# Kernel optimization log

Hardware: AMD Instinct MI355X
Metric: run time of the kernel (lower is better)

Reference implementation:

```python
import jax, jax.numpy as jnp
import numpy as np

B, T, C, H = 8, 1024, 1024, 16
Dh = C // H
EPS = 1e-5


def layernorm(x, g, b):
    m = jnp.mean(x, axis=-1, keepdims=True)
    v = jnp.mean((x - m) ** 2, axis=-1, keepdims=True)
    return g * (x - m) / jnp.sqrt(v + EPS) + b


def setup_inputs() -> dict:
    key = jax.random.key(0)
    ks = jax.random.split(key, 10)
    s = 0.02
    return {
        "x": jax.random.normal(ks[0], (B, T, C), jnp.float32),
        "Wq": jax.random.normal(ks[1], (H, C, Dh), jnp.float32) * s,
        "Wk": jax.random.normal(ks[2], (H, C, Dh), jnp.float32) * s,
        "Wv": jax.random.normal(ks[3], (H, C, Dh), jnp.float32) * s,
        "Wproj": jax.random.normal(ks[4], (C, C), jnp.float32) * s,
        "bproj": jnp.zeros((C,), jnp.float32),
        "W1": jax.random.normal(ks[5], (C, C), jnp.float32) * s,
        "b1": jnp.zeros((C,), jnp.float32),
        "W2": jax.random.normal(ks[6], (C, C), jnp.float32) * s,
        "b2": jnp.zeros((C,), jnp.float32),
        "g1": jnp.ones((C,), jnp.float32),
        "beta1": jnp.zeros((C,), jnp.float32),
        "g2": jnp.ones((C,), jnp.float32),
        "beta2": jnp.zeros((C,), jnp.float32),
    }


def reference(x, Wq, Wk, Wv, Wproj, bproj, W1, b1, W2, b2, g1, beta1, g2, beta2):
    # pre-LN multi-head causal self-attention + residual
    xn = layernorm(x, g1, beta1)
    q = jnp.einsum("btc,hcd->bhtd", xn, Wq)
    k = jnp.einsum("btc,hcd->bhtd", xn, Wk)
    v = jnp.einsum("btc,hcd->bhtd", xn, Wv)
    scores = jnp.einsum("bhtd,bhsd->bhts", q, k) * (Dh ** -0.5)
    causal = jnp.tril(jnp.ones((T, T), bool))  # [T,T]
    scores = jnp.where(causal, scores, -jnp.inf)
    wei = jax.nn.softmax(scores, axis=-1)
    attn = jnp.einsum("bhts,bhsd->bhtd", wei, v)
    attn = attn.transpose(0, 2, 1, 3).reshape(B, T, C)  # concat heads
    x = x + attn @ Wproj + bproj
    # pre-LN MLP (n_emb -> n_emb, ReLU, n_emb -> n_emb) + residual
    xn2 = layernorm(x, g2, beta2)
    h = jax.nn.relu(xn2 @ W1 + b1)
    x = x + h @ W2 + b2
    return x
```

## Files before the change

kernel.cpp:

```cpp
#include <hip/hip_runtime.h>
#include <hip/hip_bf16.h>

#define KDIM 1024

typedef __bf16  bf16x8  __attribute__((ext_vector_type(8)));
typedef float   floatx4 __attribute__((ext_vector_type(4)));

__device__ inline short f2bf(float f) {
    unsigned u = __float_as_uint(f);
    u += 0x7fffu + ((u >> 16) & 1u);
    return (short)(u >> 16);
}
__device__ inline float bf2f(short s) {
    return __uint_as_float(((unsigned)(unsigned short)s) << 16);
}
__device__ inline unsigned pk2bf(float x, float y) {
    __hip_bfloat162 h = __float22bfloat162_rn(make_float2(x, y));
    return *reinterpret_cast<unsigned*>(&h);
}
__device__ inline float exp2_hw(float x) {
    float r;
    __asm__("v_exp_f32 %0, %1" : "=v"(r) : "v"(x));
    return r;
}

__device__ inline floatx4 mfma16(bf16x8 a, bf16x8 b, floatx4 c) {
    return __builtin_amdgcn_mfma_f32_16x16x32_bf16(a, b, c, 0, 0, 0);
}

__device__ inline void load_lds16(const void* g, void* l) {
    __builtin_amdgcn_global_load_lds(
        (__attribute__((address_space(1))) void*)(unsigned long long)g,
        (__attribute__((address_space(3))) void*)(unsigned)(unsigned long long)l,
        16, 0, 0);
}

template <bool BF16IN>
__global__ __launch_bounds__(256) void ln_kernel(
    const void* __restrict__ xv, const float* __restrict__ g,
    const float* __restrict__ be, short* __restrict__ out)
{
    const int row = blockIdx.x, tid = threadIdx.x;
    float4 v;
    if constexpr (BF16IN) {
        const short4 s4 = ((const short4*)xv)[(size_t)row * 256 + tid];
        v.x = bf2f(s4.x); v.y = bf2f(s4.y); v.z = bf2f(s4.z); v.w = bf2f(s4.w);
    } else {
        v = ((const float4*)xv)[(size_t)row * 256 + tid];
    }
    float s  = v.x + v.y + v.z + v.w;
    float s2 = v.x * v.x + v.y * v.y + v.z * v.z + v.w * v.w;
    #pragma unroll
    for (int off = 32; off; off >>= 1) {
        s  += __shfl_down(s, off);
        s2 += __shfl_down(s2, off);
    }
    __shared__ float red1[4], red2[4];
    const int w = tid >> 6, lane = tid & 63;
    if (lane == 0) { red1[w] = s; red2[w] = s2; }
    __syncthreads();
    s  = red1[0] + red1[1] + red1[2] + red1[3];
    s2 = red2[0] + red2[1] + red2[2] + red2[3];
    const float mean = s * (1.0f / 1024.0f);
    const float var  = s2 * (1.0f / 1024.0f) - mean * mean;
    const float rstd = rsqrtf(var + 1e-5f);
    const float4 gg = ((const float4*)g)[tid];
    const float4 bb = ((const float4*)be)[tid];
    const unsigned o01 = pk2bf((v.x - mean) * rstd * gg.x + bb.x,
                               (v.y - mean) * rstd * gg.y + bb.y);
    const unsigned o23 = pk2bf((v.z - mean) * rstd * gg.z + bb.z,
                               (v.w - mean) * rstd * gg.w + bb.w);
    *(uint2*)(out + (size_t)row * 1024 + tid * 4) = make_uint2(o01, o23);
}

__global__ void pack_all(const float* __restrict__ Wq, const float* __restrict__ Wk,
                         const float* __restrict__ Wv, const float* __restrict__ Wproj,
                         const float* __restrict__ W1, const float* __restrict__ W2,
                         short* __restrict__ qkvT, short* __restrict__ projT,
                         short* __restrict__ w1T, short* __restrict__ w2T)
{
    __shared__ float tile[32][33];
    const int bx = blockIdx.x, c0 = blockIdx.y * 32;
    const int tx = threadIdx.x, ty = threadIdx.y;
    if (bx < 96) {
        const int n0 = bx * 32;
        const int grp = n0 >> 10;
        const float* W = (grp == 0) ? Wq : (grp == 1 ? Wk : Wv);
        const int nb = n0 & 1023, hh = nb >> 6, d0 = nb & 63;
        #pragma unroll
        for (int j = 0; j < 32; j += 8)
            tile[ty + j][tx] = W[hh * 65536 + (c0 + ty + j) * 64 + d0 + tx];
        __syncthreads();
        #pragma unroll
        for (int j = 0; j < 32; j += 8)
            qkvT[(size_t)(n0 + ty + j) * 1024 + c0 + tx] = f2bf(tile[tx][ty + j]);
    } else {
        const int which = (bx - 96) >> 5;
        const int n0 = ((bx - 96) & 31) * 32;
        const float* src = (which == 0) ? Wproj : (which == 1 ? W1 : W2);
        short* dst = (which == 0) ? projT : (which == 1 ? w1T : w2T);
        #pragma unroll
        for (int j = 0; j < 32; j += 8)
            tile[ty + j][tx] = src[(size_t)(c0 + ty + j) * 1024 + n0 + tx];
        __syncthreads();
        #pragma unroll
        for (int j = 0; j < 32; j += 8)
            dst[(size_t)(n0 + ty + j) * 1024 + c0 + tx] = f2bf(tile[tx][ty + j]);
    }
}

template <int EPI, bool SWAP>
__global__ __launch_bounds__(256, 4) void gemm_bt(
    const short* __restrict__ A, const short* __restrict__ BT, int N,
    const float* __restrict__ bias, const float* __restrict__ residF,
    const short* __restrict__ residH,
    float* __restrict__ outF, short* __restrict__ outH,
    short* __restrict__ qO, short* __restrict__ kO, short* __restrict__ vtO)
{
    const int tid = threadIdx.x, lane = tid & 63, w = tid >> 6;
    const int wm = w >> 1, wn = w & 1;
    const int mi = lane & 15, quad = lane >> 4;
    const int lid = blockIdx.x + gridDim.x * blockIdx.y;
    const int xcd = lid & 7, i8 = lid >> 3;
    const int rowBase = (xcd * 8 + (i8 & 7)) * 128;
    const int colBase = (i8 >> 3) * 128;

    __shared__ alignas(16) short As[2][128 * 32];
    __shared__ alignas(16) short Bs[2][128 * 32];

    const floatx4 z4 = {0.f, 0.f, 0.f, 0.f};
    floatx4 acc[4][4];
    #pragma unroll
    for (int i = 0; i < 4; ++i)
        #pragma unroll
        for (int j = 0; j < 4; ++j) acc[i][j] = z4;

    auto stage = [&](int k0, int buf) {
        #pragma unroll
        for (int i = 0; i < 2; ++i) {
            const int cb = i * 256 + w * 64;
            const int chunk = cb + lane;
            const int r = chunk >> 2, cc = chunk & 3;
            const int csw = cc ^ ((r >> 1) & 3);
            load_lds16(A + (size_t)(rowBase + r) * KDIM + k0 + csw * 8,
                       (char*)As[buf] + cb * 16);
            load_lds16(BT + (size_t)(colBase + r) * KDIM + k0 + csw * 8,
                       (char*)Bs[buf] + cb * 16);
        }
    };

    auto compute = [&](const short* Ac, const short* Bc) {
        bf16x8 af[4], bfv[4];
        #pragma unroll
        for (int it = 0; it < 4; ++it) {
            const int ra = wm * 64 + it * 16 + mi;
            af[it] = *(const bf16x8*)(Ac + ra * 32 + ((quad ^ ((ra >> 1) & 3)) << 3));
        }
        #pragma unroll
        for (int jt = 0; jt < 4; ++jt) {
            const int rb = wn * 64 + jt * 16 + mi;
            bfv[jt] = *(const bf16x8*)(Bc + rb * 32 + ((quad ^ ((rb >> 1) & 3)) << 3));
        }
        #pragma unroll
        for (int it = 0; it < 4; ++it)
            #pragma unroll
            for (int jt = 0; jt < 4; ++jt) {
                if constexpr (SWAP)
                    acc[it][jt] = mfma16(bfv[jt], af[it], acc[it][jt]);
                else
                    acc[it][jt] = mfma16(af[it], bfv[jt], acc[it][jt]);
            }
    };

    stage(0, 0);
    #pragma unroll 1
    for (int c = 0; c < KDIM / 32; c += 2) {
        __syncthreads();
        if (c + 1 < KDIM / 32) stage((c + 1) * 32, 1);
        compute(As[0], Bs[0]);
        __syncthreads();
        if (c + 2 < KDIM / 32) stage((c + 2) * 32, 0);
        compute(As[1], Bs[1]);
    }

    if constexpr (SWAP) {
        #pragma unroll
        for (int it = 0; it < 4; ++it) {
            const int row = rowBase + wm * 64 + it * 16 + mi;
            #pragma unroll
            for (int jt = 0; jt < 4; ++jt) {
                const int col0 = colBase + wn * 64 + jt * 16 + quad * 4;
                const floatx4 a4 = acc[it][jt];
                if constexpr (EPI == 0) {
                    if (colBase < 1024) {
                        const float qs = 0.18033688011112042f;
                        *(uint2*)(qO + (size_t)row * 1024 + col0) =
                            make_uint2(pk2bf(a4[0] * qs, a4[1] * qs),
                                       pk2bf(a4[2] * qs, a4[3] * qs));
                    } else {
                        *(uint2*)(kO + (size_t)row * 1024 + (col0 - 1024)) =
                            make_uint2(pk2bf(a4[0], a4[1]), pk2bf(a4[2], a4[3]));
                    }
                } else if constexpr (EPI == 2) {
                    const float4 b4 = *(const float4*)(bias + col0);
                    *(uint2*)(outH + (size_t)row * N + col0) =
                        make_uint2(pk2bf(fmaxf(a4[0] + b4.x, 0.f), fmaxf(a4[1] + b4.y, 0.f)),
                                   pk2bf(fmaxf(a4[2] + b4.z, 0.f), fmaxf(a4[3] + b4.w, 0.f)));
                } else if constexpr (EPI == 4) {
                    const float4 b4 = *(const float4*)(bias + col0);
                    const float4 r4 = *(const float4*)(residF + (size_t)row * N + col0);
                    *(uint2*)(outH + (size_t)row * N + col0) =
                        make_uint2(pk2bf(a4[0] + b4.x + r4.x, a4[1] + b4.y + r4.y),
                                   pk2bf(a4[2] + b4.z + r4.z, a4[3] + b4.w + r4.w));
                } else {
                    const float4 b4 = *(const float4*)(bias + col0);
                    const short4 r4 = *(const short4*)(residH + (size_t)row * N + col0);
                    float4 o;
                    o.x = a4[0] + b4.x + bf2f(r4.x);
                    o.y = a4[1] + b4.y + bf2f(r4.y);
                    o.z = a4[2] + b4.z + bf2f(r4.z);
                    o.w = a4[3] + b4.w + bf2f(r4.w);
                    *(float4*)(outF + (size_t)row * N + col0) = o;
                }
            }
        }
    } else {
        #pragma unroll
        for (int it = 0; it < 4; ++it) {
            const int row0 = rowBase + wm * 64 + it * 16 + quad * 4;
            const int bb = row0 >> 10, t0 = row0 & 1023;
            #pragma unroll
            for (int jt = 0; jt < 4; ++jt) {
                const int c = colBase + wn * 64 + jt * 16 + mi;
                const floatx4 a4 = acc[it][jt];
                *(uint2*)(vtO + ((size_t)bb << 20) + ((size_t)c << 10) + t0) =
                    make_uint2(pk2bf(a4[0], a4[1]), pk2bf(a4[2], a4[3]));
            }
        }
    }
}

#define PSTR 88
__device__ __forceinline__ void attn_qk_pv(
    const bf16x8 qf0, const bf16x8 qf1,
    floatx4 (&o)[4], float (&lsum)[4],
    const short* Ks, const short* Vs, short* myP,
    const int mi, const int quad, const int kq, const int diagRowOff)
{
    const floatx4 z4 = {0.f, 0.f, 0.f, 0.f};
    const bool diag = diagRowOff >= 0;
    floatx4 sa[4];
    #pragma unroll
    for (int j = 0; j < 4; ++j) {
        const int row = j * 16 + mi;
        const int sw = row & 7;
        floatx4 s4 = z4;
        s4 = mfma16(qf0, *(const bf16x8*)(Ks + row * 64 + ((quad ^ sw) << 3)), s4);
        s4 = mfma16(qf1, *(const bf16x8*)(Ks + row * 64 + (((quad + 4) ^ sw) << 3)), s4);
        sa[j] = s4;
    }
    #pragma unroll
    for (int j = 0; j < 4; ++j) {
        float p[4];
        #pragma unroll
        for (int r = 0; r < 4; ++r) {
            p[r] = exp2_hw(sa[j][r]);
            if (diag && (j * 16 + mi > diagRowOff + quad * 4 + r)) p[r] = 0.f;
            lsum[r] += p[r];
        }
        const unsigned ua = pk2bf(p[0], p[1]);
        const unsigned ub = pk2bf(p[2], p[3]);
        myP[(quad * 4 + 0) * PSTR + j * 16 + mi] = (short)ua;
        myP[(quad * 4 + 1) * PSTR + j * 16 + mi] = (short)(ua >> 16);
        myP[(quad * 4 + 2) * PSTR + j * 16 + mi] = (short)ub;
        myP[(quad * 4 + 3) * PSTR + j * 16 + mi] = (short)(ub >> 16);
    }
    __asm__ volatile("s_waitcnt lgkmcnt(0)" ::: "memory");
    const bf16x8 pf0 = *(const bf16x8*)(myP + mi * PSTR + kq);
    const bf16x8 pf1 = *(const bf16x8*)(myP + mi * PSTR + 32 + kq);
    #pragma unroll
    for (int d = 0; d < 4; ++d) {
        const int row = d * 16 + mi;
        const int sw = row & 7;
        o[d] = mfma16(pf0, *(const bf16x8*)(Vs + row * 64 + ((quad ^ sw) << 3)), o[d]);
        o[d] = mfma16(pf1, *(const bf16x8*)(Vs + row * 64 + (((quad + 4) ^ sw) << 3)), o[d]);
    }
}

__global__ __launch_bounds__(256, 4) void flash_attn(
    const short* __restrict__ Q, const short* __restrict__ K,
    const short* __restrict__ Vt, short* __restrict__ O)
{
    const int tid = threadIdx.x, lane = tid & 63, w = tid >> 6;
    const int mi = lane & 15, quad = lane >> 4, kq = quad * 8;
    const int lid = blockIdx.x;
    const int xcd = lid & 7, i8 = lid >> 3;
    const int bh = xcd * 16 + (i8 & 15);
    const int pi = i8 >> 4;
    const int h = bh & 15, b = bh >> 4;
    const int tA = pi, tB = 15 - pi;
    const int qbA = tA * 64, qbB = tB * 64;

    __shared__ alignas(16) short Ks[64 * 64];
    __shared__ alignas(16) short Vs[64 * 64];
    __shared__ alignas(16) short Ps[4][16 * PSTR];

    const size_t qoffA = ((size_t)(b * 1024 + qbA + w * 16 + mi)) * 1024 + h * 64;
    const size_t qoffB = ((size_t)(b * 1024 + qbB + w * 16 + mi)) * 1024 + h * 64;
    const bf16x8 qA0 = *(const bf16x8*)(Q + qoffA + kq);
    const bf16x8 qA1 = *(const bf16x8*)(Q + qoffA + 32 + kq);
    const bf16x8 qB0 = *(const bf16x8*)(Q + qoffB + kq);
    const bf16x8 qB1 = *(const bf16x8*)(Q + qoffB + 32 + kq);

    const floatx4 z4 = {0.f, 0.f, 0.f, 0.f};
    floatx4 oA[4], oB[4];
    float lA[4], lB[4];
    #pragma unroll
    for (int i = 0; i < 4; ++i) { oA[i] = z4; oB[i] = z4; lA[i] = 0.f; lB[i] = 0.f; }

    short* myP = &Ps[w][0];
    for (int t = 0; t <= tB; ++t) {
        const int s0 = t * 64;
        __syncthreads();
        #pragma unroll
        for (int i = 0; i < 2; ++i) {
            const int cb = i * 256 + w * 64;
            const int chunk = cb + lane;
            const int r = chunk >> 3, c = chunk & 7;
            const int csw = c ^ (r & 7);
            load_lds16(K + ((size_t)(b * 1024 + s0 + r)) * 1024 + h * 64 + csw * 8,
                       (char*)Ks + cb * 16);
            load_lds16(Vt + ((size_t)b << 20) + ((size_t)(h * 64 + r) << 10) + s0 + csw * 8,
                       (char*)Vs + cb * 16);
        }
        __syncthreads();

        if (t <= tA)
            attn_qk_pv(qA0, qA1, oA, lA, Ks, Vs, myP, mi, quad, kq,
                       (t == tA) ? (w * 16) : -1);
        attn_qk_pv(qB0, qB1, oB, lB, Ks, Vs, myP, mi, quad, kq,
                   (t == tB) ? (w * 16) : -1);
    }

    #pragma unroll
    for (int r = 0; r < 4; ++r) {
        float sA = lA[r], sB = lB[r];
        #pragma unroll
        for (int off = 1; off < 16; off <<= 1) {
            sA += __shfl_xor(sA, off);
            sB += __shfl_xor(sB, off);
        }
        lA[r] = 1.0f / sA;
        lB[r] = 1.0f / sB;
    }
    #pragma unroll
    for (int d = 0; d < 4; ++d)
        #pragma unroll
        for (int r = 0; r < 4; ++r) {
            const int col = h * 64 + d * 16 + mi;
            const int rowA = b * 1024 + qbA + w * 16 + quad * 4 + r;
            const int rowB = b * 1024 + qbB + w * 16 + quad * 4 + r;
            O[(size_t)rowA * 1024 + col] = f2bf(oA[d][r] * lA[r]);
            O[(size_t)rowB * 1024 + col] = f2bf(oB[d][r] * lB[r]);
        }
}

extern "C" void kernel_launch(void* const* d_in, const int* in_sizes, int n_in,
                              void* d_out, int out_size, void* d_ws, size_t ws_size,
                              hipStream_t stream)
{
    (void)in_sizes; (void)n_in; (void)out_size; (void)ws_size;
    const float* x     = (const float*)d_in[0];
    const float* Wq    = (const float*)d_in[1];
    const float* Wk    = (const float*)d_in[2];
    const float* Wv    = (const float*)d_in[3];
    const float* Wproj = (const float*)d_in[4];
    const float* bproj = (const float*)d_in[5];
    const float* W1    = (const float*)d_in[6];
    const float* b1    = (const float*)d_in[7];
    const float* W2    = (const float*)d_in[8];
    const float* b2    = (const float*)d_in[9];
    const float* g1    = (const float*)d_in[10];
    const float* be1   = (const float*)d_in[11];
    const float* g2    = (const float*)d_in[12];
    const float* be2   = (const float*)d_in[13];
    float* out = (float*)d_out;

    char* ws = (char*)d_ws;
    const size_t MB = 1u << 20;
    short* Qb     = (short*)(ws + 0 * MB);
    short* Kb     = (short*)(ws + 16 * MB);
    short* Vtb    = (short*)(ws + 32 * MB);
    short* XN     = (short*)(ws + 48 * MB);
    short* AT     = (short*)(ws + 64 * MB);
    short* R2b    = (short*)(ws + 80 * MB);
    short* WqkvT  = (short*)(ws + 112 * MB);
    short* WprojT = (short*)(ws + 118 * MB);
    short* W1T    = (short*)(ws + 120 * MB);
    short* W2T    = (short*)(ws + 122 * MB);

    pack_all<<<dim3(192, 32), dim3(32, 8), 0, stream>>>(
        Wq, Wk, Wv, Wproj, W1, W2, WqkvT, WprojT, W1T, W2T);

    ln_kernel<false><<<8192, 256, 0, stream>>>(x, g1, be1, XN);

    gemm_bt<0, true><<<dim3(16, 64), 256, 0, stream>>>(XN, WqkvT, 1024,
        nullptr, nullptr, nullptr, nullptr, nullptr, Qb, Kb, nullptr);
    gemm_bt<3, false><<<dim3(8, 64), 256, 0, stream>>>(XN, WqkvT + 2048 * KDIM, 1024,
        nullptr, nullptr, nullptr, nullptr, nullptr, nullptr, nullptr, Vtb);

    flash_attn<<<1024, 256, 0, stream>>>(Qb, Kb, Vtb, AT);

    gemm_bt<4, true><<<dim3(8, 64), 256, 0, stream>>>(AT, WprojT, 1024,
        bproj, x, nullptr, nullptr, R2b, nullptr, nullptr, nullptr);

    ln_kernel<true><<<8192, 256, 0, stream>>>(R2b, g2, be2, XN);

    gemm_bt<2, true><<<dim3(8, 64), 256, 0, stream>>>(XN, W1T, 1024,
        b1, nullptr, nullptr, nullptr, AT, nullptr, nullptr, nullptr);

    gemm_bt<5, true><<<dim3(8, 64), 256, 0, stream>>>(AT, W2T, 1024,
        b2, nullptr, R2b, out, nullptr, nullptr, nullptr, nullptr);
}
```

Baseline: 314.8 us.

## Merge pack and LN1 kernels, fuse QKV GEMMs, use 8-wave blocks for N=1024 GEMMs

Folds the weight pack/transpose and the first layernorm into one launch, and merges the Q/K and V GEMMs into a single 1536-block launch. This cuts launch count and the tail effects between kernels. The three N=1024 GEMMs now use 512-thread blocks with 8 waves, each wave owning 32x64 of the 128x128 tile, so more waves per CU are available to hide latency. The cost is fewer accumulators per wave, which lowers MFMA reuse of the LDS fragments.

New measurement: 306.0 us. 2.8% less time.

```diff
diff --git a/kernel.cpp b/kernel.cpp
--- a/kernel.cpp
+++ b/kernel.cpp
@@ -36,11 +36,11 @@
 }
 
 template <bool BF16IN>
-__global__ __launch_bounds__(256) void ln_kernel(
+__device__ __forceinline__ void ln_body(
     const void* __restrict__ xv, const float* __restrict__ g,
-    const float* __restrict__ be, short* __restrict__ out)
-{
-    const int row = blockIdx.x, tid = threadIdx.x;
+    const float* __restrict__ be, short* __restrict__ out,
+    const int row, const int tid)
+{
     float4 v;
     if constexpr (BF16IN) {
         const short4 s4 = ((const short4*)xv)[(size_t)row * 256 + tid];
@@ -73,15 +73,31 @@
     *(uint2*)(out + (size_t)row * 1024 + tid * 4) = make_uint2(o01, o23);
 }
 
-__global__ void pack_all(const float* __restrict__ Wq, const float* __restrict__ Wk,
-                         const float* __restrict__ Wv, const float* __restrict__ Wproj,
-                         const float* __restrict__ W1, const float* __restrict__ W2,
-                         short* __restrict__ qkvT, short* __restrict__ projT,
-                         short* __restrict__ w1T, short* __restrict__ w2T)
-{
+__global__ __launch_bounds__(256) void ln_kernel_bf16(
+    const short* __restrict__ xv, const float* __restrict__ g,
+    const float* __restrict__ be, short* __restrict__ out)
+{
+    ln_body<true>(xv, g, be, out, blockIdx.x, threadIdx.x);
+}
+
+__global__ __launch_bounds__(256) void pre_kernel(
+    const float* __restrict__ x, const float* __restrict__ g1,
+    const float* __restrict__ be1, short* __restrict__ XN,
+    const float* __restrict__ Wq, const float* __restrict__ Wk,
+    const float* __restrict__ Wv, const float* __restrict__ Wproj,
+    const float* __restrict__ W1, const float* __restrict__ W2,
+    short* __restrict__ qkvT, short* __restrict__ projT,
+    short* __restrict__ w1T, short* __restrict__ w2T)
+{
+    const int id = blockIdx.x, tid = threadIdx.x;
+    if (id < 8192) {
+        ln_body<false>(x, g1, be1, XN, id, tid);
+        return;
+    }
     __shared__ float tile[32][33];
-    const int bx = blockIdx.x, c0 = blockIdx.y * 32;
-    const int tx = threadIdx.x, ty = threadIdx.y;
+    const int pidx = id - 8192;
+    const int bx = pidx % 192, c0 = (pidx / 192) * 32;
+    const int tx = tid & 31, ty = tid >> 5;
     if (bx < 96) {
         const int n0 = bx * 32;
         const int grp = n0 >> 10;
@@ -109,36 +125,18 @@
     }
 }
 
-template <int EPI, bool SWAP>
-__global__ __launch_bounds__(256, 4) void gemm_bt(
-    const short* __restrict__ A, const short* __restrict__ BT, int N,
-    const float* __restrict__ bias, const float* __restrict__ residF,
-    const short* __restrict__ residH,
-    float* __restrict__ outF, short* __restrict__ outH,
-    short* __restrict__ qO, short* __restrict__ kO, short* __restrict__ vtO)
-{
-    const int tid = threadIdx.x, lane = tid & 63, w = tid >> 6;
+template <bool SWAP, int WAVES, int IT>
+__device__ __forceinline__ void kloop(
+    const short* __restrict__ A, const short* __restrict__ BT,
+    short (&As)[2][128 * 32], short (&Bs)[2][128 * 32],
+    floatx4 (&acc)[IT][4], const int rowBase, const int colBase,
+    const int w, const int lane, const int mi, const int quad)
+{
     const int wm = w >> 1, wn = w & 1;
-    const int mi = lane & 15, quad = lane >> 4;
-    const int lid = blockIdx.x + gridDim.x * blockIdx.y;
-    const int xcd = lid & 7, i8 = lid >> 3;
-    const int rowBase = (xcd * 8 + (i8 & 7)) * 128;
-    const int colBase = (i8 >> 3) * 128;
-
-    __shared__ alignas(16) short As[2][128 * 32];
-    __shared__ alignas(16) short Bs[2][128 * 32];
-
-    const floatx4 z4 = {0.f, 0.f, 0.f, 0.f};
-    floatx4 acc[4][4];
-    #pragma unroll
-    for (int i = 0; i < 4; ++i)
-        #pragma unroll
-        for (int j = 0; j < 4; ++j) acc[i][j] = z4;
-
     auto stage = [&](int k0, int buf) {
         #pragma unroll
-        for (int i = 0; i < 2; ++i) {
-            const int cb = i * 256 + w * 64;
+        for (int i = 0; i < 512 / (WAVES * 64); ++i) {
+            const int cb = i * (WAVES * 64) + w * 64;
             const int chunk = cb + lane;
             const int r = chunk >> 2, cc = chunk & 3;
             const int csw = cc ^ ((r >> 1) & 3);
@@ -148,12 +146,11 @@
                        (char*)Bs[buf] + cb * 16);
         }
     };
-
     auto compute = [&](const short* Ac, const short* Bc) {
-        bf16x8 af[4], bfv[4];
-        #pragma unroll
-        for (int it = 0; it < 4; ++it) {
-            const int ra = wm * 64 + it * 16 + mi;
+        bf16x8 af[IT], bfv[4];
+        #pragma unroll
+        for (int it = 0; it < IT; ++it) {
+            const int ra = wm * (IT * 16) + it * 16 + mi;
             af[it] = *(const bf16x8*)(Ac + ra * 32 + ((quad ^ ((ra >> 1) & 3)) << 3));
         }
         #pragma unroll
@@ -162,7 +159,7 @@
             bfv[jt] = *(const bf16x8*)(Bc + rb * 32 + ((quad ^ ((rb >> 1) & 3)) << 3));
         }
         #pragma unroll
-        for (int it = 0; it < 4; ++it)
+        for (int it = 0; it < IT; ++it)
             #pragma unroll
             for (int jt = 0; jt < 4; ++jt) {
                 if constexpr (SWAP)
@@ -171,7 +168,6 @@
                     acc[it][jt] = mfma16(af[it], bfv[jt], acc[it][jt]);
             }
     };
-
     stage(0, 0);
     #pragma unroll 1
     for (int c = 0; c < KDIM / 32; c += 2) {
@@ -182,8 +178,32 @@
         if (c + 2 < KDIM / 32) stage((c + 2) * 32, 0);
         compute(As[1], Bs[1]);
     }
-
-    if constexpr (SWAP) {
+}
+
+__global__ __launch_bounds__(256, 4) void gemm_qkv(
+    const short* __restrict__ XN, const short* __restrict__ WT,
+    short* __restrict__ qO, short* __restrict__ kO, short* __restrict__ vtO)
+{
+    const int tid = threadIdx.x, lane = tid & 63, w = tid >> 6;
+    const int mi = lane & 15, quad = lane >> 4;
+    const int lid = blockIdx.x;
+    const int xcd = lid & 7, i8 = lid >> 3;
+    const int rowBase = (xcd * 8 + (i8 & 7)) * 128;
+    const int colBase = (i8 >> 3) * 128;
+
+    __shared__ alignas(16) short As[2][128 * 32];
+    __shared__ alignas(16) short Bs[2][128 * 32];
+
+    const floatx4 z4 = {0.f, 0.f, 0.f, 0.f};
+    const int wm = w >> 1, wn = w & 1;
+
+    if (colBase < 2048) {
+        floatx4 acc[4][4];
+        #pragma unroll
+        for (int i = 0; i < 4; ++i)
+            #pragma unroll
+            for (int j = 0; j < 4; ++j) acc[i][j] = z4;
+        kloop<true, 4, 4>(XN, WT, As, Bs, acc, rowBase, colBase, w, lane, mi, quad);
         #pragma unroll
         for (int it = 0; it < 4; ++it) {
             const int row = rowBase + wm * 64 + it * 16 + mi;
@@ -191,50 +211,93 @@
             for (int jt = 0; jt < 4; ++jt) {
                 const int col0 = colBase + wn * 64 + jt * 16 + quad * 4;
                 const floatx4 a4 = acc[it][jt];
-                if constexpr (EPI == 0) {
-                    if (colBase < 1024) {
-                        const float qs = 0.18033688011112042f;
-                        *(uint2*)(qO + (size_t)row * 1024 + col0) =
-                            make_uint2(pk2bf(a4[0] * qs, a4[1] * qs),
-                                       pk2bf(a4[2] * qs, a4[3] * qs));
-                    } else {
-                        *(uint2*)(kO + (size_t)row * 1024 + (col0 - 1024)) =
-                            make_uint2(pk2bf(a4[0], a4[1]), pk2bf(a4[2], a4[3]));
-                    }
-                } else if constexpr (EPI == 2) {
-                    const float4 b4 = *(const float4*)(bias + col0);
-                    *(uint2*)(outH + (size_t)row * N + col0) =
-                        make_uint2(pk2bf(fmaxf(a4[0] + b4.x, 0.f), fmaxf(a4[1] + b4.y, 0.f)),
-                                   pk2bf(fmaxf(a4[2] + b4.z, 0.f), fmaxf(a4[3] + b4.w, 0.f)));
-                } else if constexpr (EPI == 4) {
-                    const float4 b4 = *(const float4*)(bias + col0);
-                    const float4 r4 = *(const float4*)(residF + (size_t)row * N + col0);
-                    *(uint2*)(outH + (size_t)row * N + col0) =
-                        make_uint2(pk2bf(a4[0] + b4.x + r4.x, a4[1] + b4.y + r4.y),
-                                   pk2bf(a4[2] + b4.z + r4.z, a4[3] + b4.w + r4.w));
+                if (colBase < 1024) {
+                    const float qs = 0.18033688011112042f;
+                    *(uint2*)(qO + (size_t)row * 1024 + col0) =
+                        make_uint2(pk2bf(a4[0] * qs, a4[1] * qs),
+                                   pk2bf(a4[2] * qs, a4[3] * qs));
                 } else {
-                    const float4 b4 = *(const float4*)(bias + col0);
-                    const short4 r4 = *(const short4*)(residH + (size_t)row * N + col0);
-                    float4 o;
-                    o.x = a4[0] + b4.x + bf2f(r4.x);
-                    o.y = a4[1] + b4.y + bf2f(r4.y);
-                    o.z = a4[2] + b4.z + bf2f(r4.z);
-                    o.w = a4[3] + b4.w + bf2f(r4.w);
-                    *(float4*)(outF + (size_t)row * N + col0) = o;
+                    *(uint2*)(kO + (size_t)row * 1024 + (col0 - 1024)) =
+                        make_uint2(pk2bf(a4[0], a4[1]), pk2bf(a4[2], a4[3]));
                 }
             }
         }
     } else {
+        floatx4 acc[4][4];
+        #pragma unroll
+        for (int i = 0; i < 4; ++i)
+            #pragma unroll
+            for (int j = 0; j < 4; ++j) acc[i][j] = z4;
+        kloop<false, 4, 4>(XN, WT, As, Bs, acc, rowBase, colBase, w, lane, mi, quad);
         #pragma unroll
         for (int it = 0; it < 4; ++it) {
             const int row0 = rowBase + wm * 64 + it * 16 + quad * 4;
             const int bb = row0 >> 10, t0 = row0 & 1023;
             #pragma unroll
             for (int jt = 0; jt < 4; ++jt) {
-                const int c = colBase + wn * 64 + jt * 16 + mi;
+                const int c = (colBase - 2048) + wn * 64 + jt * 16 + mi;
                 const floatx4 a4 = acc[it][jt];
                 *(uint2*)(vtO + ((size_t)bb << 20) + ((size_t)c << 10) + t0) =
                     make_uint2(pk2bf(a4[0], a4[1]), pk2bf(a4[2], a4[3]));
+            }
+        }
+    }
+}
+
+template <int EPI>
+__global__ __launch_bounds__(512, 2) void gemm_n1024(
+    const short* __restrict__ A, const short* __restrict__ BT,
+    const float* __restrict__ bias, const float* __restrict__ residF,
+    const short* __restrict__ residH,
+    float* __restrict__ outF, short* __restrict__ outH)
+{
+    const int tid = threadIdx.x, lane = tid & 63, w = tid >> 6;
+    const int mi = lane & 15, quad = lane >> 4;
+    const int lid = blockIdx.x;
+    const int xcd = lid & 7, i8 = lid >> 3;
+    const int rowBase = (xcd * 8 + (i8 & 7)) * 128;
+    const int colBase = (i8 >> 3) * 128;
+
+    __shared__ alignas(16) short As[2][128 * 32];
+    __shared__ alignas(16) short Bs[2][128 * 32];
+
+    const floatx4 z4 = {0.f, 0.f, 0.f, 0.f};
+    floatx4 acc[2][4];
+    #pragma unroll
+    for (int i = 0; i < 2; ++i)
+        #pragma unroll
+        for (int j = 0; j < 4; ++j) acc[i][j] = z4;
+
+    kloop<true, 8, 2>(A, BT, As, Bs, acc, rowBase, colBase, w, lane, mi, quad);
+
+    const int wm = w >> 1, wn = w & 1;
+    #pragma unroll
+    for (int it = 0; it < 2; ++it) {
+        const int row = rowBase + wm * 32 + it * 16 + mi;
+        #pragma unroll
+        for (int jt = 0; jt < 4; ++jt) {
+            const int col0 = colBase + wn * 64 + jt * 16 + quad * 4;
+            const floatx4 a4 = acc[it][jt];
+            if constexpr (EPI == 2) {
+                const float4 b4 = *(const float4*)(bias + col0);
+                *(uint2*)(outH + (size_t)row * 1024 + col0) =
+                    make_uint2(pk2bf(fmaxf(a4[0] + b4.x, 0.f), fmaxf(a4[1] + b4.y, 0.f)),
+                               pk2bf(fmaxf(a4[2] + b4.z, 0.f), fmaxf(a4[3] + b4.w, 0.f)));
+            } else if constexpr (EPI == 4) {
+                const float4 b4 = *(const float4*)(bias + col0);
+                const float4 r4 = *(const float4*)(residF + (size_t)row * 1024 + col0);
+                *(uint2*)(outH + (size_t)row * 1024 + col0) =
+                    make_uint2(pk2bf(a4[0] + b4.x + r4.x, a4[1] + b4.y + r4.y),
+                               pk2bf(a4[2] + b4.z + r4.z, a4[3] + b4.w + r4.w));
+            } else {
+                const float4 b4 = *(const float4*)(bias + col0);
+                const short4 r4 = *(const short4*)(residH + (size_t)row * 1024 + col0);
+                float4 o;
+                o.x = a4[0] + b4.x + bf2f(r4.x);
+                o.y = a4[1] + b4.y + bf2f(r4.y);
+                o.z = a4[2] + b4.z + bf2f(r4.z);
+                o.w = a4[3] + b4.w + bf2f(r4.w);
+                *(float4*)(outF + (size_t)row * 1024 + col0) = o;
             }
         }
     }
@@ -399,26 +462,21 @@
     short* W1T    = (short*)(ws + 120 * MB);
     short* W2T    = (short*)(ws + 122 * MB);
 
-    pack_all<<<dim3(192, 32), dim3(32, 8), 0, stream>>>(
-        Wq, Wk, Wv, Wproj, W1, W2, WqkvT, WprojT, W1T, W2T);
-
-    ln_kernel<false><<<8192, 256, 0, stream>>>(x, g1, be1, XN);
-
-    gemm_bt<0, true><<<dim3(16, 64), 256, 0, stream>>>(XN, WqkvT, 1024,
-        nullptr, nullptr, nullptr, nullptr, nullptr, Qb, Kb, nullptr);
-    gemm_bt<3, false><<<dim3(8, 64), 256, 0, stream>>>(XN, WqkvT + 2048 * KDIM, 1024,
-        nullptr, nullptr, nullptr, nullptr, nullptr, nullptr, nullptr, Vtb);
+    pre_kernel<<<8192 + 6144, 256, 0, stream>>>(
+        x, g1, be1, XN, Wq, Wk, Wv, Wproj, W1, W2, WqkvT, WprojT, W1T, W2T);
+
+    gemm_qkv<<<1536, 256, 0, stream>>>(XN, WqkvT, Qb, Kb, Vtb);
 
     flash_attn<<<1024, 256, 0, stream>>>(Qb, Kb, Vtb, AT);
 
-    gemm_bt<4, true><<<dim3(8, 64), 256, 0, stream>>>(AT, WprojT, 1024,
-        bproj, x, nullptr, nullptr, R2b, nullptr, nullptr, nullptr);
-
-    ln_kernel<true><<<8192, 256, 0, stream>>>(R2b, g2, be2, XN);
-
-    gemm_bt<2, true><<<dim3(8, 64), 256, 0, stream>>>(XN, W1T, 1024,
-        b1, nullptr, nullptr, nullptr, AT, nullptr, nullptr, nullptr);
-
-    gemm_bt<5, true><<<dim3(8, 64), 256, 0, stream>>>(AT, W2T, 1024,
-        b2, nullptr, R2b, out, nullptr, nullptr, nullptr, nullptr);
-}
+    gemm_n1024<4><<<512, 512, 0, stream>>>(AT, WprojT, bproj, x, nullptr,
+                                           nullptr, R2b);
+
+    ln_kernel_bf16<<<8192, 256, 0, stream>>>(R2b, g2, be2, XN);
+
+    gemm_n1024<2><<<512, 512, 0, stream>>>(XN, W1T, b1, nullptr, nullptr,
+                                           nullptr, AT);
+
+    gemm_n1024<5><<<512, 512, 0, stream>>>(AT, W2T, b2, nullptr, R2b,
+                                           out, nullptr);
+}
```
